# Performance work log

Hardware: AMD Instinct MI355X
Metric: run time of the kernel (lower is better)

The kernel has to match this reference:

```python
import jax, jax.numpy as jnp
import numpy as np

HIDDEN = 2048
LATENT = 512
ROPE_DIM = 64
NUM_HEADS = 16
HEAD_DIM = HIDDEN // NUM_HEADS  # 128
ROPE_THETA = 10000.0
B, S = 2, 2048


def _rope_tables(seq_len):
    # theta_i = 1 / rope_theta ** (2i / rope_dim)
    theta = 1.0 / ROPE_THETA ** (jnp.arange(0, ROPE_DIM, 2, dtype=jnp.float32) / ROPE_DIM)
    idx_theta = jnp.arange(seq_len, dtype=jnp.float32)[:, None] * theta[None, :]  # [S, rd/2]
    return jnp.cos(idx_theta), jnp.sin(idx_theta)


def _apply_rope(x, cos, sin):
    # x: [B, S, H, rd]; interleaved pairs rotated, matching the torch RoPE module.
    x2 = x.reshape(*x.shape[:-1], -1, 2)  # [B,S,H,rd/2,2]
    c = cos[None, :, None, :]
    s = sin[None, :, None, :]
    out = jnp.stack([x2[..., 0] * c - x2[..., 1] * s,
                     x2[..., 1] * c + x2[..., 0] * s], axis=-1)
    return out.reshape(x.shape)


def setup_inputs() -> dict:
    key = jax.random.key(0)
    ks = jax.random.split(key, 9)
    def lin(k, fan_in, fan_out):
        # weights stored [in, out]; y = x @ W (same math as torch Linear)
        bound = 1.0 / np.sqrt(fan_in)
        return jax.random.uniform(k, (fan_in, fan_out), jnp.float32, -bound, bound)
    return {
        "h": jax.random.normal(ks[0], (B, S, HIDDEN), jnp.float32),
        "W_DKV": lin(ks[1], HIDDEN, LATENT),
        "W_UK": lin(ks[2], LATENT, HIDDEN),
        "W_KR": lin(ks[3], HIDDEN, ROPE_DIM),
        "W_UV": lin(ks[4], LATENT, HIDDEN),
        "W_DQ": lin(ks[5], HIDDEN, LATENT),
        "W_UQ": lin(ks[6], LATENT, HIDDEN),
        "W_QR": lin(ks[7], LATENT, ROPE_DIM * NUM_HEADS),
        "W_O": lin(ks[8], HIDDEN, HIDDEN),
    }


def reference(h, W_DKV, W_UK, W_KR, W_UV, W_DQ, W_UQ, W_QR, W_O):
    b, s, _ = h.shape
    cos, sin = _rope_tables(s)

    # --- keys / values (shared latent) ---
    c_KV = h @ W_DKV                                      # [B,S,latent]
    k_C = (c_KV @ W_UK).reshape(b, s, NUM_HEADS, HEAD_DIM)
    k_R = _apply_rope((h @ W_KR)[:, :, None, :], cos, sin)  # [B,S,1,rd]
    k_R = jnp.broadcast_to(k_R, (b, s, NUM_HEADS, ROPE_DIM))
    k = jnp.concatenate([k_C, k_R], axis=-1)             # [B,S,H,hd+rd]
    v = (c_KV @ W_UV).reshape(b, s, NUM_HEADS, HEAD_DIM)

    # --- queries ---
    c_Q = h @ W_DQ                                        # [B,S,latent]
    q_C = (c_Q @ W_UQ).reshape(b, s, NUM_HEADS, HEAD_DIM)
    q_R = _apply_rope((c_Q @ W_QR).reshape(b, s, NUM_HEADS, ROPE_DIM), cos, sin)
    q = jnp.concatenate([q_C, q_R], axis=-1)             # [B,S,H,hd+rd]

    # --- attention (explicit SxS scores, causal) ---
    scale = 1.0 / np.sqrt(HEAD_DIM + ROPE_DIM)
    scores = jnp.einsum('bshd,bthd->bhst', q, k) * scale  # [B,H,S,S]
    causal = jnp.tril(jnp.ones((s, s), dtype=bool))
    scores = jnp.where(causal[None, None], scores, -jnp.inf)
    probs = jax.nn.softmax(scores, axis=-1)
    o = jnp.einsum('bhst,bthd->bshd', probs, v)           # [B,S,H,hd]

    return o.reshape(b, s, HIDDEN) @ W_O
```

## Files before the change

kernel.cpp:

```cpp
#include <hip/hip_runtime.h>
#include <hip/hip_bf16.h>
#include <type_traits>
#include <cstdint>

typedef __bf16 bf16x8 __attribute__((ext_vector_type(8)));
typedef float f32x4 __attribute__((ext_vector_type(4)));
typedef __hip_bfloat16 bf16;

static constexpr int BB = 2, SEQ = 2048, HID = 2048, LAT = 512, NHEAD = 16;
static constexpr int HD = 128, RD = 64, DQK = 192;
static constexpr int MR = BB * SEQ;
static constexpr int LDW1 = 1152;
static constexpr int LDKV = 4096;
static constexpr int LDQ3 = 3072;

__device__ __forceinline__ float bf2f(bf16 x) { return __bfloat162float(x); }
__device__ __forceinline__ bf16 f2bf(float x) { return __float2bfloat16(x); }

__device__ __forceinline__ void gload16(const void* g, void* l) {
  __builtin_amdgcn_global_load_lds(
      (__attribute__((address_space(1))) void*)(uintptr_t)g,
      (__attribute__((address_space(3))) void*)(uint32_t)(uintptr_t)l,
      16, 0, 0);
}

__global__ void k_prep(const float* __restrict__ h,
                       const float* __restrict__ Wdkv, const float* __restrict__ Wdq,
                       const float* __restrict__ Wkr, const float* __restrict__ Wuk,
                       const float* __restrict__ Wuv, const float* __restrict__ Wuq,
                       const float* __restrict__ Wqr, const float* __restrict__ Wo,
                       bf16* __restrict__ hb, bf16* __restrict__ wt1, bf16* __restrict__ wt2,
                       bf16* __restrict__ wt3, bf16* __restrict__ woT,
                       float* __restrict__ cosT, float* __restrict__ sinT) {
  __shared__ float tbuf[32][33];
  int blk = blockIdx.x;
  if (blk >= 10112) {
    int i = (blk - 10112) * 256 + threadIdx.x;
    float4 v = reinterpret_cast<const float4*>(h)[i];
    bf16* o = hb + (size_t)i * 4;
    o[0] = f2bf(v.x); o[1] = f2bf(v.y); o[2] = f2bf(v.z); o[3] = f2bf(v.w);
    return;
  }
  if (blk >= 9856) {
    int idx = (blk - 9856) * 256 + threadIdx.x;
    int s = idx >> 5, j = idx & 31;
    float freq = powf(10000.0f, -(float)(2 * j) / 64.0f);
    float a = (float)s * freq;
    cosT[idx] = cosf(a);
    sinT[idx] = sinf(a);
    return;
  }
  const float* src; bf16* dst; int K, N, local;
  if (blk < 1024)      { src = Wdkv; dst = wt1;                      K = 2048; N = 512;  local = blk; }
  else if (blk < 2048) { src = Wdq;  dst = wt1 + (size_t)512 * 2048; K = 2048; N = 512;  local = blk - 1024; }
  else if (blk < 2176) { src = Wkr;  dst = wt1 + (size_t)1024 * 2048;K = 2048; N = 64;   local = blk - 2048; }
  else if (blk < 3200) { src = Wuk;  dst = wt2;                      K = 512;  N = 2048; local = blk - 2176; }
  else if (blk < 4224) { src = Wuv;  dst = wt2 + (size_t)2048 * 512; K = 512;  N = 2048; local = blk - 3200; }
  else if (blk < 5248) { src = Wuq;  dst = wt3;                      K = 512;  N = 2048; local = blk - 4224; }
  else if (blk < 5760) { src = Wqr;  dst = wt3 + (size_t)2048 * 512; K = 512;  N = 1024; local = blk - 5248; }
  else                 { src = Wo;   dst = woT;                      K = 2048; N = 2048; local = blk - 5760; }
  int tilesX = N >> 5;
  int tx = local % tilesX, ty = local / tilesX;
  int k0 = ty * 32, n0 = tx * 32;
  int c = threadIdx.x & 31, r0 = threadIdx.x >> 5;
#pragma unroll
  for (int i = 0; i < 32; i += 8) tbuf[r0 + i][c] = src[(size_t)(k0 + r0 + i) * N + n0 + c];
  __syncthreads();
#pragma unroll
  for (int i = 0; i < 32; i += 8)
    dst[(size_t)(n0 + r0 + i) * K + k0 + c] = f2bf(tbuf[c][r0 + i]);
}

template <int BM, int BN, typename OutT>
__device__ __forceinline__ void gemm_body(const bf16* __restrict__ A, int lda,
                                          const bf16* __restrict__ BT,
                                          OutT* __restrict__ C, int ldc, int K,
                                          int m0, int n0) {
  constexpr int BK = 32;
  constexpr int WN = BN / 64, NW = (BM / 64) * WN;
  __shared__ alignas(16) bf16 As[BM * BK];
  __shared__ alignas(16) bf16 Bs[BN * BK];
  const int tid = threadIdx.x, wave = tid >> 6, lane = tid & 63;
  const int lr = lane & 15, lk = lane >> 4;
  const int wm = (wave / WN) * 64, wn = (wave % WN) * 64;
  const int srow = lane >> 2;
  const int scol = (lane & 3) * 8;
  f32x4 acc[4][4] = {};
  for (int kt = 0; kt < K; kt += BK) {
    for (int c = wave; c < BM / 16; c += NW)
      gload16(A + (size_t)(m0 + c * 16 + srow) * lda + kt + scol, (char*)As + c * 1024);
    for (int c = wave; c < BN / 16; c += NW)
      gload16(BT + (size_t)(n0 + c * 16 + srow) * K + kt + scol, (char*)Bs + c * 1024);
    __syncthreads();
    bf16x8 af[4], bfr[4];
#pragma unroll
    for (int i = 0; i < 4; i++)
      af[i] = *reinterpret_cast<const bf16x8*>(As + (wm + i * 16 + lr) * BK + lk * 8);
#pragma unroll
    for (int j = 0; j < 4; j++)
      bfr[j] = *reinterpret_cast<const bf16x8*>(Bs + (wn + j * 16 + lr) * BK + lk * 8);
    __builtin_amdgcn_s_setprio(1);
#pragma unroll
    for (int i = 0; i < 4; i++)
#pragma unroll
      for (int j = 0; j < 4; j++)
        acc[i][j] = __builtin_amdgcn_mfma_f32_16x16x32_bf16(af[i], bfr[j], acc[i][j], 0, 0, 0);
    __builtin_amdgcn_s_setprio(0);
    __syncthreads();
  }
#pragma unroll
  for (int i = 0; i < 4; i++)
#pragma unroll
    for (int j = 0; j < 4; j++) {
      int row = m0 + wm + i * 16 + lk * 4, col = n0 + wn + j * 16 + lr;
#pragma unroll
      for (int r = 0; r < 4; r++) {
        float v = acc[i][j][r];
        if constexpr (std::is_same<OutT, float>::value)
          C[(size_t)(row + r) * ldc + col] = v;
        else
          C[(size_t)(row + r) * ldc + col] = f2bf(v);
      }
    }
}

template <int BM, int BN, typename OutT>
__global__ __launch_bounds__(256)
void k_gemm_bt(const bf16* __restrict__ A, int lda, const bf16* __restrict__ BT,
               OutT* __restrict__ C, int ldc, int K) {
  gemm_body<BM, BN, OutT>(A, lda, BT, C, ldc, K, blockIdx.y * BM, blockIdx.x * BN);
}

__global__ __launch_bounds__(256)
void k_gemm23(const bf16* __restrict__ out1, const bf16* __restrict__ wt2,
              const bf16* __restrict__ wt3, bf16* __restrict__ kv, bf16* __restrict__ q3) {
  int n0g = blockIdx.x * 128, m0 = blockIdx.y * 128;
  const bf16* A; const bf16* BT; bf16* C; int ldc, n0;
  if (n0g < LDKV) { A = out1;       BT = wt2; C = kv; ldc = LDKV; n0 = n0g; }
  else            { A = out1 + 512; BT = wt3; C = q3; ldc = LDQ3; n0 = n0g - LDKV; }
  gemm_body<128, 128, bf16>(A, LDW1, BT, C, ldc, LAT, m0, n0);
}

__device__ __forceinline__ bf16x8 rope8(bf16x8 x, float4 c4, float4 s4) {
  bf16x8 o;
  float cp[4] = {c4.x, c4.y, c4.z, c4.w};
  float sp[4] = {s4.x, s4.y, s4.z, s4.w};
#pragma unroll
  for (int pe = 0; pe < 4; pe++) {
    float x0 = (float)x[2 * pe], x1 = (float)x[2 * pe + 1];
    o[2 * pe]     = (__bf16)(x0 * cp[pe] - x1 * sp[pe]);
    o[2 * pe + 1] = (__bf16)(x1 * cp[pe] + x0 * sp[pe]);
  }
  return o;
}

__global__ void k_assemble(const bf16* __restrict__ q3, const bf16* __restrict__ kv,
                           const bf16* __restrict__ out1,
                           const float* __restrict__ cosT, const float* __restrict__ sinT,
                           bf16* __restrict__ qbuf, bf16* __restrict__ kbuf,
                           bf16* __restrict__ vt) {
  __shared__ bf16 tv[32][34];
  int blk = blockIdx.x;
  if (blk < 12288) {
    bool isQ = blk < 6144;
    int gid = (isQ ? blk : blk - 6144) * 256 + threadIdx.x;
    int rowIdx = gid / 24, pos = gid - rowIdx * 24;
    int d8 = pos * 8;
    int s = rowIdx & (SEQ - 1);
    int bhh = rowIdx >> 11;
    int hh = bhh & 15, b = bhh >> 4;
    size_t row = (size_t)b * SEQ + s;
    bf16x8 o;
    if (isQ) {
      if (d8 < HD) {
        o = *reinterpret_cast<const bf16x8*>(&q3[row * LDQ3 + hh * HD + d8]);
      } else {
        int dd8 = d8 - HD;
        bf16x8 x = *reinterpret_cast<const bf16x8*>(&q3[row * LDQ3 + HID + hh * RD + dd8]);
        float4 c4 = *reinterpret_cast<const float4*>(&cosT[s * 32 + (dd8 >> 1)]);
        float4 s4 = *reinterpret_cast<const float4*>(&sinT[s * 32 + (dd8 >> 1)]);
        o = rope8(x, c4, s4);
      }
      *reinterpret_cast<bf16x8*>(&qbuf[(size_t)gid * 8]) = o;
    } else {
      if (d8 < HD) {
        o = *reinterpret_cast<const bf16x8*>(&kv[row * LDKV + hh * HD + d8]);
      } else {
        int dd8 = d8 - HD;
        bf16x8 x = *reinterpret_cast<const bf16x8*>(&out1[row * LDW1 + 1024 + dd8]);
        float4 c4 = *reinterpret_cast<const float4*>(&cosT[s * 32 + (dd8 >> 1)]);
        float4 s4 = *reinterpret_cast<const float4*>(&sinT[s * 32 + (dd8 >> 1)]);
        o = rope8(x, c4, s4);
      }
      *reinterpret_cast<bf16x8*>(&kbuf[(size_t)gid * 8]) = o;
    }
    return;
  }
  int local = blk - 12288;
  int dx = local & 3, sy = (local >> 2) & 63, bh = local >> 8;
  int b = bh >> 4, hh = bh & 15;
  int s0 = sy * 32, d0 = dx * 32;
  int c = threadIdx.x & 31, r0 = threadIdx.x >> 5;
#pragma unroll
  for (int i = 0; i < 32; i += 8)
    tv[r0 + i][c] = kv[((size_t)b * SEQ + s0 + r0 + i) * LDKV + HID + hh * HD + d0 + c];
  __syncthreads();
#pragma unroll
  for (int i = 0; i < 32; i += 8)
    vt[((size_t)bh * HD + d0 + r0 + i) * SEQ + s0 + c] = tv[c][r0 + i];
}

__global__ __launch_bounds__(256)
void k_attn(const bf16* __restrict__ Q, const bf16* __restrict__ Kb,
            const bf16* __restrict__ VT, bf16* __restrict__ Of) {
  constexpr int KBL = 64, NT = SEQ / 64;
  __shared__ alignas(16) bf16 Ks[KBL * DQK];
  __shared__ alignas(16) bf16 Vs[HD * KBL];
  __shared__ alignas(16) bf16 Ps[4 * 16 * KBL];
  const int nid = (blockIdx.x & 7) * 64 + (blockIdx.x >> 3);
  const int bh = nid >> 4, pid = nid & 15;
  const int qtA = pid, qtB = NT - 1 - pid;
  const int b = bh >> 4, hh = bh & 15;
  const int tid = threadIdx.x, wave = tid >> 6, lane = tid & 63;
  const int lr = lane & 15, lk = lane >> 4;
  const int rb = wave * 16 + lk * 4;
  const float scale = 0.07216878364870323f;

  bf16x8 qf[2][6];
#pragma unroll
  for (int t = 0; t < 2; t++) {
    int q0 = (t ? qtB : qtA) * 64;
    const bf16* Qp = Q + ((size_t)bh * SEQ + q0 + wave * 16 + lr) * DQK;
#pragma unroll
    for (int c = 0; c < 6; c++)
      qf[t][c] = *reinterpret_cast<const bf16x8*>(Qp + c * 32 + lk * 8);
  }

  bf16* PsW = Ps + wave * (16 * KBL);
  f32x4 oacc[2][8] = {};
  float mrow[2][4], lrow[2][4];
#pragma unroll
  for (int t = 0; t < 2; t++)
#pragma unroll
    for (int r = 0; r < 4; r++) { mrow[t][r] = -INFINITY; lrow[t][r] = 0.f; }

  auto proc = [&](auto tc, bool maskit, int k0, int q0) {
    constexpr int t = decltype(tc)::value;
    f32x4 sc[4] = {};
    __builtin_amdgcn_s_setprio(1);
#pragma unroll
    for (int cb = 0; cb < 4; cb++) {
      const int krow = cb * 16 + lr;
#pragma unroll
      for (int c = 0; c < 6; c++) {
        int phys = (c * 4 + lk) ^ (krow & 7);
        bf16x8 kf = *reinterpret_cast<const bf16x8*>(Ks + krow * DQK + phys * 8);
        sc[cb] = __builtin_amdgcn_mfma_f32_16x16x32_bf16(qf[t][c], kf, sc[cb], 0, 0, 0);
      }
    }
    __builtin_amdgcn_s_setprio(0);
    float p[4][4], tm[4];
#pragma unroll
    for (int r = 0; r < 4; r++) tm[r] = -INFINITY;
#pragma unroll
    for (int cb = 0; cb < 4; cb++) {
      const int kcg = k0 + cb * 16 + lr;
#pragma unroll
      for (int r = 0; r < 4; r++) {
        float v = sc[cb][r] * scale;
        if (maskit && kcg > q0 + rb + r) v = -INFINITY;
        p[cb][r] = v;
        tm[r] = fmaxf(tm[r], v);
      }
    }
#pragma unroll
    for (int m = 1; m < 16; m <<= 1)
#pragma unroll
      for (int r = 0; r < 4; r++) tm[r] = fmaxf(tm[r], __shfl_xor(tm[r], m, 16));
    float rs[4];
#pragma unroll
    for (int r = 0; r < 4; r++) {
      float mo = mrow[t][r];
      float mn = fmaxf(mo, tm[r]);
      if (tm[r] > mo) {
        float al = __expf(mo - mn);
        mrow[t][r] = mn;
        lrow[t][r] *= al;
#pragma unroll
        for (int ocb = 0; ocb < 8; ocb++) oacc[t][ocb][r] *= al;
      }
      float ssum = 0.f;
#pragma unroll
      for (int cb = 0; cb < 4; cb++) {
        float e = __expf(p[cb][r] - mn);
        p[cb][r] = e;
        ssum += e;
      }
      rs[r] = ssum;
    }
#pragma unroll
    for (int m = 1; m < 16; m <<= 1)
#pragma unroll
      for (int r = 0; r < 4; r++) rs[r] += __shfl_xor(rs[r], m, 16);
#pragma unroll
    for (int r = 0; r < 4; r++) lrow[t][r] += rs[r];
#pragma unroll
    for (int cb = 0; cb < 4; cb++)
#pragma unroll
      for (int r = 0; r < 4; r++) {
        int prow = lk * 4 + r;
        int pslot = (cb * 2 + (lr >> 3)) ^ (prow & 7);
        PsW[prow * KBL + pslot * 8 + (lr & 7)] = f2bf(p[cb][r]);
      }
    __builtin_amdgcn_s_setprio(1);
#pragma unroll
    for (int kk = 0; kk < 2; kk++) {
      int pphys = (kk * 4 + lk) ^ (lr & 7);
      bf16x8 pa = *reinterpret_cast<const bf16x8*>(PsW + lr * KBL + pphys * 8);
#pragma unroll
      for (int ocb = 0; ocb < 8; ocb++) {
        int vrow = ocb * 16 + lr;
        int vphys = (kk * 4 + lk) ^ (vrow & 7);
        bf16x8 vb = *reinterpret_cast<const bf16x8*>(Vs + vrow * KBL + vphys * 8);
        oacc[t][ocb] = __builtin_amdgcn_mfma_f32_16x16x32_bf16(pa, vb, oacc[t][ocb], 0, 0, 0);
      }
    }
    __builtin_amdgcn_s_setprio(0);
  };

  for (int kt = 0; kt <= qtB; kt++) {
    const int k0 = kt * KBL;
    const bf16* Kbase = Kb + ((size_t)bh * SEQ + k0) * DQK;
    const bf16* Vbase = VT + (size_t)bh * HD * SEQ + k0;
    for (int c = wave; c < 24; c += 4) {
      int S = c * 64 + lane;
      int row = S / 24;
      int scl = (S - row * 24) ^ (row & 7);
      gload16(Kbase + row * DQK + scl * 8, (char*)Ks + c * 1024);
    }
    for (int c = wave; c < 16; c += 4) {
      int S = c * 64 + lane;
      int row = S >> 3;
      int scl = (S & 7) ^ (row & 7);
      gload16(Vbase + (size_t)row * SEQ + scl * 8, (char*)Vs + c * 1024);
    }
    __syncthreads();
    proc(std::integral_constant<int, 1>{}, kt == qtB, k0, qtB * 64);
    if (kt <= qtA) proc(std::integral_constant<int, 0>{}, kt == qtA, k0, qtA * 64);
    __syncthreads();
  }

#pragma unroll
  for (int t = 0; t < 2; t++) {
    int q0 = (t ? qtB : qtA) * 64;
#pragma unroll
    for (int ocb = 0; ocb < 8; ocb++)
#pragma unroll
      for (int r = 0; r < 4; r++) {
        int qr = q0 + rb + r;
        float v = oacc[t][ocb][r] / lrow[t][r];
        Of[((size_t)b * SEQ + qr) * HID + hh * HD + ocb * 16 + lr] = f2bf(v);
      }
  }
}

extern "C" void kernel_launch(void* const* d_in, const int* in_sizes, int n_in,
                              void* d_out, int out_size, void* d_ws, size_t ws_size,
                              hipStream_t stream) {
  const float* h    = (const float*)d_in[0];
  const float* Wdkv = (const float*)d_in[1];
  const float* Wuk  = (const float*)d_in[2];
  const float* Wkr  = (const float*)d_in[3];
  const float* Wuv  = (const float*)d_in[4];
  const float* Wdq  = (const float*)d_in[5];
  const float* Wuq  = (const float*)d_in[6];
  const float* Wqr  = (const float*)d_in[7];
  const float* Wo   = (const float*)d_in[8];
  float* out = (float*)d_out;

  char* w = (char*)d_ws;
  auto alloc = [&](size_t elems) {
    bf16* p = (bf16*)w;
    w += (elems * sizeof(bf16) + 255) & ~(size_t)255;
    return p;
  };
  bf16* hb   = alloc((size_t)MR * HID);
  bf16* wt1  = alloc((size_t)LDW1 * HID);
  bf16* wt2  = alloc((size_t)LDKV * LAT);
  bf16* wt3  = alloc((size_t)LDQ3 * LAT);
  bf16* woT  = alloc((size_t)HID * HID);
  bf16* out1 = alloc((size_t)MR * LDW1);
  bf16* kv   = alloc((size_t)MR * LDKV);
  bf16* q3   = alloc((size_t)MR * LDQ3);
  bf16* qbuf = alloc((size_t)BB * NHEAD * SEQ * DQK);
  bf16* kbuf = alloc((size_t)BB * NHEAD * SEQ * DQK);
  bf16* vt   = alloc((size_t)BB * NHEAD * HD * SEQ);
  bf16* oflat= alloc((size_t)MR * HID);
  float* cosT = (float*)alloc((size_t)SEQ * 32 * 2);
  float* sinT = (float*)alloc((size_t)SEQ * 32 * 2);

  k_prep<<<18304, 256, 0, stream>>>(h, Wdkv, Wdq, Wkr, Wuk, Wuv, Wuq, Wqr, Wo,
                                    hb, wt1, wt2, wt3, woT, cosT, sinT);
  k_gemm_bt<128, 128, bf16><<<dim3(LDW1 / 128, MR / 128), 256, 0, stream>>>(hb, HID, wt1, out1, LDW1, HID);
  k_gemm23<<<dim3((LDKV + LDQ3) / 128, MR / 128), 256, 0, stream>>>(out1, wt2, wt3, kv, q3);
  k_assemble<<<20480, 256, 0, stream>>>(q3, kv, out1, cosT, sinT, qbuf, kbuf, vt);
  k_attn<<<512, 256, 0, stream>>>(qbuf, kbuf, vt, oflat);
  k_gemm_bt<128, 128, float><<<dim3(HID / 128, MR / 128), 256, 0, stream>>>(oflat, HID, woT, out, HID, HID);
}
```

Before: 501.3 us.

## Restructure causal attention: one query tile per block, double-buffered 32-key tiles

Replaces the paired-query-tile scheme, where each block handled tiles qtA and qtB to balance causal work, with one 64-row query tile per block. Blocks are launched in order of descending work, so the grid grows from 512 to 1024 blocks. Key tiles shrink from 64 to 32 and are double-buffered in LDS: the next tile's global-to-LDS load is issued before computing on the current one, replacing the two barriers per iteration with one. The V tile uses a padded row stride (80 bytes) in place of an XOR swizzle. The intent is to hide load latency and raise occupancy. The cost is more iterations, each with less MFMA work, and more per-tile softmax overhead.

```diff
diff --git a/kernel.cpp b/kernel.cpp
--- a/kernel.cpp
+++ b/kernel.cpp
@@ -213,57 +213,81 @@
 __global__ __launch_bounds__(256)
 void k_attn(const bf16* __restrict__ Q, const bf16* __restrict__ Kb,
             const bf16* __restrict__ VT, bf16* __restrict__ Of) {
-  constexpr int KBL = 64, NT = SEQ / 64;
-  __shared__ alignas(16) bf16 Ks[KBL * DQK];
-  __shared__ alignas(16) bf16 Vs[HD * KBL];
-  __shared__ alignas(16) bf16 Ps[4 * 16 * KBL];
-  const int nid = (blockIdx.x & 7) * 64 + (blockIdx.x >> 3);
-  const int bh = nid >> 4, pid = nid & 15;
-  const int qtA = pid, qtB = NT - 1 - pid;
+  constexpr int QB = 64, KBL = 32;
+  __shared__ alignas(16) bf16 Ks[2][KBL * DQK];
+  __shared__ alignas(16) bf16 Vs[2][HD * 40];
+  __shared__ alignas(16) bf16 Ps[4][16 * KBL];
+  const int qt = (SEQ / QB - 1) - (blockIdx.x >> 5);
+  const int bh = blockIdx.x & 31;
   const int b = bh >> 4, hh = bh & 15;
   const int tid = threadIdx.x, wave = tid >> 6, lane = tid & 63;
   const int lr = lane & 15, lk = lane >> 4;
+  const int q0 = qt * QB;
   const int rb = wave * 16 + lk * 4;
   const float scale = 0.07216878364870323f;
 
-  bf16x8 qf[2][6];
-#pragma unroll
-  for (int t = 0; t < 2; t++) {
-    int q0 = (t ? qtB : qtA) * 64;
-    const bf16* Qp = Q + ((size_t)bh * SEQ + q0 + wave * 16 + lr) * DQK;
-#pragma unroll
-    for (int c = 0; c < 6; c++)
-      qf[t][c] = *reinterpret_cast<const bf16x8*>(Qp + c * 32 + lk * 8);
-  }
-
-  bf16* PsW = Ps + wave * (16 * KBL);
-  f32x4 oacc[2][8] = {};
-  float mrow[2][4], lrow[2][4];
-#pragma unroll
-  for (int t = 0; t < 2; t++)
-#pragma unroll
-    for (int r = 0; r < 4; r++) { mrow[t][r] = -INFINITY; lrow[t][r] = 0.f; }
-
-  auto proc = [&](auto tc, bool maskit, int k0, int q0) {
-    constexpr int t = decltype(tc)::value;
-    f32x4 sc[4] = {};
+  const bf16* Qp = Q + ((size_t)bh * SEQ + q0 + wave * 16 + lr) * DQK;
+  bf16x8 qf[6];
+#pragma unroll
+  for (int c = 0; c < 6; c++)
+    qf[c] = *reinterpret_cast<const bf16x8*>(Qp + c * 32 + lk * 8);
+
+  bf16* PsW = Ps[wave];
+  const bf16* Kbh = Kb + (size_t)bh * SEQ * DQK;
+  const bf16* Vbh = VT + (size_t)bh * HD * SEQ;
+
+  f32x4 oacc[8] = {};
+  float mrow[4], lrow[4];
+#pragma unroll
+  for (int r = 0; r < 4; r++) { mrow[r] = -INFINITY; lrow[r] = 0.f; }
+
+  auto stage = [&](int nb, int kt) {
+    const bf16* Kbase = Kbh + (size_t)kt * KBL * DQK;
+    const bf16* Vbase = Vbh + kt * KBL;
+    for (int c = wave; c < 12; c += 4) {
+      int S = c * 64 + lane;
+      int row = S / 24;
+      int scl = (S - row * 24) ^ (row & 7);
+      gload16(Kbase + row * DQK + scl * 8, (char*)Ks[nb] + c * 1024);
+    }
+    for (int c = wave; c < 10; c += 4) {
+      int S = c * 64 + lane;
+      int row = S / 5;
+      int sl = S - row * 5;
+      gload16(Vbase + (size_t)row * SEQ + sl * 8, (char*)Vs[nb] + c * 1024);
+    }
+  };
+
+  const int ktmax = 2 * qt + 1;
+  stage(0, 0);
+  __syncthreads();
+
+  for (int kt = 0; kt <= ktmax; kt++) {
+    const int buf = kt & 1;
+    if (kt < ktmax) stage(buf ^ 1, kt + 1);
+    const int k0 = kt * KBL;
+    const bf16* Kt = Ks[buf];
+
+    f32x4 sc[2] = {};
     __builtin_amdgcn_s_setprio(1);
 #pragma unroll
-    for (int cb = 0; cb < 4; cb++) {
+    for (int cb = 0; cb < 2; cb++) {
       const int krow = cb * 16 + lr;
 #pragma unroll
       for (int c = 0; c < 6; c++) {
         int phys = (c * 4 + lk) ^ (krow & 7);
-        bf16x8 kf = *reinterpret_cast<const bf16x8*>(Ks + krow * DQK + phys * 8);
-        sc[cb] = __builtin_amdgcn_mfma_f32_16x16x32_bf16(qf[t][c], kf, sc[cb], 0, 0, 0);
+        bf16x8 kf = *reinterpret_cast<const bf16x8*>(Kt + krow * DQK + phys * 8);
+        sc[cb] = __builtin_amdgcn_mfma_f32_16x16x32_bf16(qf[c], kf, sc[cb], 0, 0, 0);
       }
     }
     __builtin_amdgcn_s_setprio(0);
-    float p[4][4], tm[4];
+
+    const bool maskit = (kt >= 2 * qt);
+    float p[2][4], tm[4];
 #pragma unroll
     for (int r = 0; r < 4; r++) tm[r] = -INFINITY;
 #pragma unroll
-    for (int cb = 0; cb < 4; cb++) {
+    for (int cb = 0; cb < 2; cb++) {
       const int kcg = k0 + cb * 16 + lr;
 #pragma unroll
       for (int r = 0; r < 4; r++) {
@@ -277,21 +301,22 @@
     for (int m = 1; m < 16; m <<= 1)
 #pragma unroll
       for (int r = 0; r < 4; r++) tm[r] = fmaxf(tm[r], __shfl_xor(tm[r], m, 16));
+
     float rs[4];
 #pragma unroll
     for (int r = 0; r < 4; r++) {
-      float mo = mrow[t][r];
+      float mo = mrow[r];
       float mn = fmaxf(mo, tm[r]);
       if (tm[r] > mo) {
         float al = __expf(mo - mn);
-        mrow[t][r] = mn;
-        lrow[t][r] *= al;
-#pragma unroll
-        for (int ocb = 0; ocb < 8; ocb++) oacc[t][ocb][r] *= al;
+        mrow[r] = mn;
+        lrow[r] *= al;
+#pragma unroll
+        for (int ocb = 0; ocb < 8; ocb++) oacc[ocb][r] *= al;
       }
       float ssum = 0.f;
 #pragma unroll
-      for (int cb = 0; cb < 4; cb++) {
+      for (int cb = 0; cb < 2; cb++) {
         float e = __expf(p[cb][r] - mn);
         p[cb][r] = e;
         ssum += e;
@@ -303,65 +328,40 @@
 #pragma unroll
       for (int r = 0; r < 4; r++) rs[r] += __shfl_xor(rs[r], m, 16);
 #pragma unroll
-    for (int r = 0; r < 4; r++) lrow[t][r] += rs[r];
-#pragma unroll
-    for (int cb = 0; cb < 4; cb++)
+    for (int r = 0; r < 4; r++) lrow[r] += rs[r];
+
+#pragma unroll
+    for (int cb = 0; cb < 2; cb++)
 #pragma unroll
       for (int r = 0; r < 4; r++) {
         int prow = lk * 4 + r;
-        int pslot = (cb * 2 + (lr >> 3)) ^ (prow & 7);
+        int pslot = (cb * 2 + (lr >> 3)) ^ r;
         PsW[prow * KBL + pslot * 8 + (lr & 7)] = f2bf(p[cb][r]);
       }
+
     __builtin_amdgcn_s_setprio(1);
-#pragma unroll
-    for (int kk = 0; kk < 2; kk++) {
-      int pphys = (kk * 4 + lk) ^ (lr & 7);
+    {
+      int pphys = lk ^ (lr & 3);
       bf16x8 pa = *reinterpret_cast<const bf16x8*>(PsW + lr * KBL + pphys * 8);
 #pragma unroll
       for (int ocb = 0; ocb < 8; ocb++) {
         int vrow = ocb * 16 + lr;
-        int vphys = (kk * 4 + lk) ^ (vrow & 7);
-        bf16x8 vb = *reinterpret_cast<const bf16x8*>(Vs + vrow * KBL + vphys * 8);
-        oacc[t][ocb] = __builtin_amdgcn_mfma_f32_16x16x32_bf16(pa, vb, oacc[t][ocb], 0, 0, 0);
+        bf16x8 vb = *reinterpret_cast<const bf16x8*>((const char*)Vs[buf] + vrow * 80 + lk * 16);
+        oacc[ocb] = __builtin_amdgcn_mfma_f32_16x16x32_bf16(pa, vb, oacc[ocb], 0, 0, 0);
       }
     }
     __builtin_amdgcn_s_setprio(0);
-  };
-
-  for (int kt = 0; kt <= qtB; kt++) {
-    const int k0 = kt * KBL;
-    const bf16* Kbase = Kb + ((size_t)bh * SEQ + k0) * DQK;
-    const bf16* Vbase = VT + (size_t)bh * HD * SEQ + k0;
-    for (int c = wave; c < 24; c += 4) {
-      int S = c * 64 + lane;
-      int row = S / 24;
-      int scl = (S - row * 24) ^ (row & 7);
-      gload16(Kbase + row * DQK + scl * 8, (char*)Ks + c * 1024);
-    }
-    for (int c = wave; c < 16; c += 4) {
-      int S = c * 64 + lane;
-      int row = S >> 3;
-      int scl = (S & 7) ^ (row & 7);
-      gload16(Vbase + (size_t)row * SEQ + scl * 8, (char*)Vs + c * 1024);
-    }
     __syncthreads();
-    proc(std::integral_constant<int, 1>{}, kt == qtB, k0, qtB * 64);
-    if (kt <= qtA) proc(std::integral_constant<int, 0>{}, kt == qtA, k0, qtA * 64);
-    __syncthreads();
-  }
-
-#pragma unroll
-  for (int t = 0; t < 2; t++) {
-    int q0 = (t ? qtB : qtA) * 64;
-#pragma unroll
-    for (int ocb = 0; ocb < 8; ocb++)
-#pragma unroll
-      for (int r = 0; r < 4; r++) {
-        int qr = q0 + rb + r;
-        float v = oacc[t][ocb][r] / lrow[t][r];
-        Of[((size_t)b * SEQ + qr) * HID + hh * HD + ocb * 16 + lr] = f2bf(v);
-      }
-  }
+  }
+
+#pragma unroll
+  for (int ocb = 0; ocb < 8; ocb++)
+#pragma unroll
+    for (int r = 0; r < 4; r++) {
+      int qr = q0 + rb + r;
+      float v = oacc[ocb][r] / lrow[r];
+      Of[((size_t)b * SEQ + qr) * HID + hh * HD + ocb * 16 + lr] = f2bf(v);
+    }
 }
 
 extern "C" void kernel_launch(void* const* d_in, const int* in_sizes, int n_in,
@@ -404,6 +404,6 @@
   k_gemm_bt<128, 128, bf16><<<dim3(LDW1 / 128, MR / 128), 256, 0, stream>>>(hb, HID, wt1, out1, LDW1, HID);
   k_gemm23<<<dim3((LDKV + LDQ3) / 128, MR / 128), 256, 0, stream>>>(out1, wt2, wt3, kv, q3);
   k_assemble<<<20480, 256, 0, stream>>>(q3, kv, out1, cosT, sinT, qbuf, kbuf, vt);
-  k_attn<<<512, 256, 0, stream>>>(qbuf, kbuf, vt, oflat);
+  k_attn<<<(SEQ / 64) * 32, 256, 0, stream>>>(qbuf, kbuf, vt, oflat);
   k_gemm_bt<128, 128, float><<<dim3(HID / 128, MR / 128), 256, 0, stream>>>(oflat, HID, woT, out, HID, HID);
 }
```

After: 476.7 us. 4.9% less time.

## Prescale Q by log2e/sqrt(d), use exp2 softmax, compute row sums via MFMA

Applied to the files above, without the earlier changes.

Folds the softmax scale and log2(e) into Q during assembly so the attention kernel uses exp2f with no per-score multiply. The row-sum reduction is replaced by an extra MFMA against a ones vector, which removes the shuffle reduction. The attention grid changes from 512 blocks, each handling a balanced pair of q-tiles, to 1024 blocks with one q-tile each, ordered longest-first. In exchange, Q is rounded to bf16 after the extra scaling, and the new grid loses the paired causal load balancing and re-reads K/V for each q-tile.

```diff
diff --git a/kernel.cpp b/kernel.cpp
--- a/kernel.cpp
+++ b/kernel.cpp
@@ -13,6 +13,7 @@
 static constexpr int LDW1 = 1152;
 static constexpr int LDKV = 4096;
 static constexpr int LDQ3 = 3072;
+static constexpr float QSC = 0.10411754f;
 
 __device__ __forceinline__ float bf2f(bf16 x) { return __bfloat162float(x); }
 __device__ __forceinline__ bf16 f2bf(float x) { return __float2bfloat16(x); }
@@ -141,15 +142,15 @@
   gemm_body<128, 128, bf16>(A, LDW1, BT, C, ldc, LAT, m0, n0);
 }
 
-__device__ __forceinline__ bf16x8 rope8(bf16x8 x, float4 c4, float4 s4) {
+__device__ __forceinline__ bf16x8 rope8(bf16x8 x, float4 c4, float4 s4, float postscale) {
   bf16x8 o;
   float cp[4] = {c4.x, c4.y, c4.z, c4.w};
   float sp[4] = {s4.x, s4.y, s4.z, s4.w};
 #pragma unroll
   for (int pe = 0; pe < 4; pe++) {
     float x0 = (float)x[2 * pe], x1 = (float)x[2 * pe + 1];
-    o[2 * pe]     = (__bf16)(x0 * cp[pe] - x1 * sp[pe]);
-    o[2 * pe + 1] = (__bf16)(x1 * cp[pe] + x0 * sp[pe]);
+    o[2 * pe]     = (__bf16)((x0 * cp[pe] - x1 * sp[pe]) * postscale);
+    o[2 * pe + 1] = (__bf16)((x1 * cp[pe] + x0 * sp[pe]) * postscale);
   }
   return o;
 }
@@ -173,13 +174,15 @@
     bf16x8 o;
     if (isQ) {
       if (d8 < HD) {
-        o = *reinterpret_cast<const bf16x8*>(&q3[row * LDQ3 + hh * HD + d8]);
+        bf16x8 x = *reinterpret_cast<const bf16x8*>(&q3[row * LDQ3 + hh * HD + d8]);
+#pragma unroll
+        for (int i = 0; i < 8; i++) o[i] = (__bf16)((float)x[i] * QSC);
       } else {
         int dd8 = d8 - HD;
         bf16x8 x = *reinterpret_cast<const bf16x8*>(&q3[row * LDQ3 + HID + hh * RD + dd8]);
         float4 c4 = *reinterpret_cast<const float4*>(&cosT[s * 32 + (dd8 >> 1)]);
         float4 s4 = *reinterpret_cast<const float4*>(&sinT[s * 32 + (dd8 >> 1)]);
-        o = rope8(x, c4, s4);
+        o = rope8(x, c4, s4, QSC);
       }
       *reinterpret_cast<bf16x8*>(&qbuf[(size_t)gid * 8]) = o;
     } else {
@@ -190,7 +193,7 @@
         bf16x8 x = *reinterpret_cast<const bf16x8*>(&out1[row * LDW1 + 1024 + dd8]);
         float4 c4 = *reinterpret_cast<const float4*>(&cosT[s * 32 + (dd8 >> 1)]);
         float4 s4 = *reinterpret_cast<const float4*>(&sinT[s * 32 + (dd8 >> 1)]);
-        o = rope8(x, c4, s4);
+        o = rope8(x, c4, s4, 1.0f);
       }
       *reinterpret_cast<bf16x8*>(&kbuf[(size_t)gid * 8]) = o;
     }
@@ -213,122 +216,39 @@
 __global__ __launch_bounds__(256)
 void k_attn(const bf16* __restrict__ Q, const bf16* __restrict__ Kb,
             const bf16* __restrict__ VT, bf16* __restrict__ Of) {
-  constexpr int KBL = 64, NT = SEQ / 64;
+  constexpr int QB = 64, KBL = 64;
   __shared__ alignas(16) bf16 Ks[KBL * DQK];
   __shared__ alignas(16) bf16 Vs[HD * KBL];
   __shared__ alignas(16) bf16 Ps[4 * 16 * KBL];
-  const int nid = (blockIdx.x & 7) * 64 + (blockIdx.x >> 3);
-  const int bh = nid >> 4, pid = nid & 15;
-  const int qtA = pid, qtB = NT - 1 - pid;
+  const int qt = (SEQ / QB - 1) - (blockIdx.x >> 5);
+  const int bh = blockIdx.x & 31;
   const int b = bh >> 4, hh = bh & 15;
   const int tid = threadIdx.x, wave = tid >> 6, lane = tid & 63;
   const int lr = lane & 15, lk = lane >> 4;
+  const int q0 = qt * QB;
   const int rb = wave * 16 + lk * 4;
-  const float scale = 0.07216878364870323f;
-
-  bf16x8 qf[2][6];
-#pragma unroll
-  for (int t = 0; t < 2; t++) {
-    int q0 = (t ? qtB : qtA) * 64;
-    const bf16* Qp = Q + ((size_t)bh * SEQ + q0 + wave * 16 + lr) * DQK;
-#pragma unroll
-    for (int c = 0; c < 6; c++)
-      qf[t][c] = *reinterpret_cast<const bf16x8*>(Qp + c * 32 + lk * 8);
+
+  const bf16* Qp = Q + ((size_t)bh * SEQ + q0 + wave * 16 + lr) * DQK;
+  bf16x8 qf[6];
+#pragma unroll
+  for (int c = 0; c < 6; c++)
+    qf[c] = *reinterpret_cast<const bf16x8*>(Qp + c * 32 + lk * 8);
+
+  bf16x8 vones = {};
+  if (lr == 0) {
+#pragma unroll
+    for (int i = 0; i < 8; i++) vones[i] = (__bf16)1.0f;
   }
 
   bf16* PsW = Ps + wave * (16 * KBL);
-  f32x4 oacc[2][8] = {};
-  float mrow[2][4], lrow[2][4];
-#pragma unroll
-  for (int t = 0; t < 2; t++)
-#pragma unroll
-    for (int r = 0; r < 4; r++) { mrow[t][r] = -INFINITY; lrow[t][r] = 0.f; }
-
-  auto proc = [&](auto tc, bool maskit, int k0, int q0) {
-    constexpr int t = decltype(tc)::value;
-    f32x4 sc[4] = {};
-    __builtin_amdgcn_s_setprio(1);
-#pragma unroll
-    for (int cb = 0; cb < 4; cb++) {
-      const int krow = cb * 16 + lr;
-#pragma unroll
-      for (int c = 0; c < 6; c++) {
-        int phys = (c * 4 + lk) ^ (krow & 7);
-        bf16x8 kf = *reinterpret_cast<const bf16x8*>(Ks + krow * DQK + phys * 8);
-        sc[cb] = __builtin_amdgcn_mfma_f32_16x16x32_bf16(qf[t][c], kf, sc[cb], 0, 0, 0);
-      }
-    }
-    __builtin_amdgcn_s_setprio(0);
-    float p[4][4], tm[4];
-#pragma unroll
-    for (int r = 0; r < 4; r++) tm[r] = -INFINITY;
-#pragma unroll
-    for (int cb = 0; cb < 4; cb++) {
-      const int kcg = k0 + cb * 16 + lr;
-#pragma unroll
-      for (int r = 0; r < 4; r++) {
-        float v = sc[cb][r] * scale;
-        if (maskit && kcg > q0 + rb + r) v = -INFINITY;
-        p[cb][r] = v;
-        tm[r] = fmaxf(tm[r], v);
-      }
-    }
-#pragma unroll
-    for (int m = 1; m < 16; m <<= 1)
-#pragma unroll
-      for (int r = 0; r < 4; r++) tm[r] = fmaxf(tm[r], __shfl_xor(tm[r], m, 16));
-    float rs[4];
-#pragma unroll
-    for (int r = 0; r < 4; r++) {
-      float mo = mrow[t][r];
-      float mn = fmaxf(mo, tm[r]);
-      if (tm[r] > mo) {
-        float al = __expf(mo - mn);
-        mrow[t][r] = mn;
-        lrow[t][r] *= al;
-#pragma unroll
-        for (int ocb = 0; ocb < 8; ocb++) oacc[t][ocb][r] *= al;
-      }
-      float ssum = 0.f;
-#pragma unroll
-      for (int cb = 0; cb < 4; cb++) {
-        float e = __expf(p[cb][r] - mn);
-        p[cb][r] = e;
-        ssum += e;
-      }
-      rs[r] = ssum;
-    }
-#pragma unroll
-    for (int m = 1; m < 16; m <<= 1)
-#pragma unroll
-      for (int r = 0; r < 4; r++) rs[r] += __shfl_xor(rs[r], m, 16);
-#pragma unroll
-    for (int r = 0; r < 4; r++) lrow[t][r] += rs[r];
-#pragma unroll
-    for (int cb = 0; cb < 4; cb++)
-#pragma unroll
-      for (int r = 0; r < 4; r++) {
-        int prow = lk * 4 + r;
-        int pslot = (cb * 2 + (lr >> 3)) ^ (prow & 7);
-        PsW[prow * KBL + pslot * 8 + (lr & 7)] = f2bf(p[cb][r]);
-      }
-    __builtin_amdgcn_s_setprio(1);
-#pragma unroll
-    for (int kk = 0; kk < 2; kk++) {
-      int pphys = (kk * 4 + lk) ^ (lr & 7);
-      bf16x8 pa = *reinterpret_cast<const bf16x8*>(PsW + lr * KBL + pphys * 8);
-#pragma unroll
-      for (int ocb = 0; ocb < 8; ocb++) {
-        int vrow = ocb * 16 + lr;
-        int vphys = (kk * 4 + lk) ^ (vrow & 7);
-        bf16x8 vb = *reinterpret_cast<const bf16x8*>(Vs + vrow * KBL + vphys * 8);
-        oacc[t][ocb] = __builtin_amdgcn_mfma_f32_16x16x32_bf16(pa, vb, oacc[t][ocb], 0, 0, 0);
-      }
-    }
-    __builtin_amdgcn_s_setprio(0);
-  };
-
-  for (int kt = 0; kt <= qtB; kt++) {
+
+  f32x4 oacc[8] = {};
+  f32x4 oaccL = {};
+  float mrow[4];
+#pragma unroll
+  for (int r = 0; r < 4; r++) mrow[r] = -INFINITY;
+
+  for (int kt = 0; kt <= qt; kt++) {
     const int k0 = kt * KBL;
     const bf16* Kbase = Kb + ((size_t)bh * SEQ + k0) * DQK;
     const bf16* Vbase = VT + (size_t)bh * HD * SEQ + k0;
@@ -345,23 +265,98 @@
       gload16(Vbase + (size_t)row * SEQ + scl * 8, (char*)Vs + c * 1024);
     }
     __syncthreads();
-    proc(std::integral_constant<int, 1>{}, kt == qtB, k0, qtB * 64);
-    if (kt <= qtA) proc(std::integral_constant<int, 0>{}, kt == qtA, k0, qtA * 64);
+
+    f32x4 sc[4] = {};
+    __builtin_amdgcn_s_setprio(1);
+#pragma unroll
+    for (int cb = 0; cb < 4; cb++) {
+      const int krow = cb * 16 + lr;
+#pragma unroll
+      for (int c = 0; c < 6; c++) {
+        int phys = (c * 4 + lk) ^ (krow & 7);
+        bf16x8 kf = *reinterpret_cast<const bf16x8*>(Ks + krow * DQK + phys * 8);
+        sc[cb] = __builtin_amdgcn_mfma_f32_16x16x32_bf16(qf[c], kf, sc[cb], 0, 0, 0);
+      }
+    }
+    __builtin_amdgcn_s_setprio(0);
+
+    const bool maskit = (kt == qt);
+    float p[4][4], tm[4];
+#pragma unroll
+    for (int r = 0; r < 4; r++) tm[r] = -INFINITY;
+#pragma unroll
+    for (int cb = 0; cb < 4; cb++) {
+      const int kcg = k0 + cb * 16 + lr;
+#pragma unroll
+      for (int r = 0; r < 4; r++) {
+        float v = sc[cb][r];
+        if (maskit && kcg > q0 + rb + r) v = -INFINITY;
+        p[cb][r] = v;
+        tm[r] = fmaxf(tm[r], v);
+      }
+    }
+#pragma unroll
+    for (int m = 1; m < 16; m <<= 1)
+#pragma unroll
+      for (int r = 0; r < 4; r++) tm[r] = fmaxf(tm[r], __shfl_xor(tm[r], m, 16));
+
+#pragma unroll
+    for (int r = 0; r < 4; r++) {
+      float mo = mrow[r];
+      float mn = fmaxf(mo, tm[r]);
+      if (tm[r] > mo) {
+        float al = exp2f(mo - mn);
+        mrow[r] = mn;
+        oaccL[r] *= al;
+#pragma unroll
+        for (int ocb = 0; ocb < 8; ocb++) oacc[ocb][r] *= al;
+      }
+#pragma unroll
+      for (int cb = 0; cb < 4; cb++) p[cb][r] = exp2f(p[cb][r] - mn);
+    }
+
+#pragma unroll
+    for (int cb = 0; cb < 4; cb++)
+#pragma unroll
+      for (int r = 0; r < 4; r++) {
+        int prow = lk * 4 + r;
+        int pslot = (cb * 2 + (lr >> 3)) ^ (prow & 7);
+        PsW[prow * KBL + pslot * 8 + (lr & 7)] = f2bf(p[cb][r]);
+      }
+
+    __builtin_amdgcn_s_setprio(1);
+#pragma unroll
+    for (int kk = 0; kk < 2; kk++) {
+      int pphys = (kk * 4 + lk) ^ (lr & 7);
+      bf16x8 pa = *reinterpret_cast<const bf16x8*>(PsW + lr * KBL + pphys * 8);
+      oaccL = __builtin_amdgcn_mfma_f32_16x16x32_bf16(pa, vones, oaccL, 0, 0, 0);
+#pragma unroll
+      for (int ocb = 0; ocb < 8; ocb++) {
+        int vrow = ocb * 16 + lr;
+        int vphys = (kk * 4 + lk) ^ (vrow & 7);
+        bf16x8 vb = *reinterpret_cast<const bf16x8*>(Vs + vrow * KBL + vphys * 8);
+        oacc[ocb] = __builtin_amdgcn_mfma_f32_16x16x32_bf16(pa, vb, oacc[ocb], 0, 0, 0);
+      }
+    }
+    __builtin_amdgcn_s_setprio(0);
     __syncthreads();
   }
 
-#pragma unroll
-  for (int t = 0; t < 2; t++) {
-    int q0 = (t ? qtB : qtA) * 64;
-#pragma unroll
-    for (int ocb = 0; ocb < 8; ocb++)
-#pragma unroll
-      for (int r = 0; r < 4; r++) {
-        int qr = q0 + rb + r;
-        float v = oacc[t][ocb][r] / lrow[t][r];
-        Of[((size_t)b * SEQ + qr) * HID + hh * HD + ocb * 16 + lr] = f2bf(v);
-      }
-  }
+  float linv[4];
+#pragma unroll
+  for (int r = 0; r < 4; r++) {
+    float l = __shfl(oaccL[r], lane & 48);
+    linv[r] = 1.0f / l;
+  }
+
+#pragma unroll
+  for (int ocb = 0; ocb < 8; ocb++)
+#pragma unroll
+    for (int r = 0; r < 4; r++) {
+      int qr = q0 + rb + r;
+      float v = oacc[ocb][r] * linv[r];
+      Of[((size_t)b * SEQ + qr) * HID + hh * HD + ocb * 16 + lr] = f2bf(v);
+    }
 }
 
 extern "C" void kernel_launch(void* const* d_in, const int* in_sizes, int n_in,
@@ -404,6 +399,6 @@
   k_gemm_bt<128, 128, bf16><<<dim3(LDW1 / 128, MR / 128), 256, 0, stream>>>(hb, HID, wt1, out1, LDW1, HID);
   k_gemm23<<<dim3((LDKV + LDQ3) / 128, MR / 128), 256, 0, stream>>>(out1, wt2, wt3, kv, q3);
   k_assemble<<<20480, 256, 0, stream>>>(q3, kv, out1, cosT, sinT, qbuf, kbuf, vt);
-  k_attn<<<512, 256, 0, stream>>>(qbuf, kbuf, vt, oflat);
+  k_attn<<<(SEQ / 64) * 32, 256, 0, stream>>>(qbuf, kbuf, vt, oflat);
   k_gemm_bt<128, 128, float><<<dim3(HID / 128, MR / 128), 256, 0, stream>>>(oflat, HID, woT, out, HID, HID);
 }
```

Measured after the change: 423.5 us. 15.5% less time.
